# Optimization experiments

Measured on AMD Instinct MI355X. Metric: run time of the kernel, lower is better.

## Reference

```python
import math
import jax, jax.numpy as jnp
import numpy as np

EMBED_LEN = 512  # self.dk in the torch module (used for scaling, NOT the head dim)


def setup_inputs() -> dict:
    key = jax.random.key(0)
    kq, kk, kv = jax.random.split(key, 3)
    B, H, S, D = 2, 8, 4096, 64
    queries = jax.random.normal(kq, (B, H, S, D), dtype=jnp.float32)
    keys = jax.random.normal(kk, (B, H, S, D), dtype=jnp.float32)
    # NOTE: values enters as [B, S, H, D]; forward transposes dims (1,2).
    values = jax.random.normal(kv, (B, S, H, D), dtype=jnp.float32)
    return {"queries": queries, "keys": keys, "values": values}


def reference(queries, keys, values):
    # compatibility = Q @ K^T / sqrt(dk), dk = embed_len (512), mask=None branch
    scores = jnp.einsum("bhqd,bhkd->bhqk", queries, keys) / math.sqrt(EMBED_LEN)
    attn = jax.nn.softmax(scores, axis=3)
    # torch.transpose(values, 1, 2): [B,S,H,D] -> [B,H,S,D]
    v = jnp.swapaxes(values, 1, 2)
    return jnp.einsum("bhqk,bhkd->bhqd", attn, v)
```

## Files before the change

### kernel.cpp

```cpp
#include <hip/hip_runtime.h>

typedef __attribute__((ext_vector_type(8))) short bf16x8;
typedef __attribute__((ext_vector_type(4))) short s16x4;
typedef __attribute__((ext_vector_type(4))) float f32x4;

#define MFMA16 __builtin_amdgcn_mfma_f32_16x16x32_bf16

#if __has_builtin(__builtin_amdgcn_exp2f)
__device__ __forceinline__ float exp2_raw(float x) { return __builtin_amdgcn_exp2f(x); }
#else
__device__ __forceinline__ float exp2_raw(float x) {
    float r;
    asm volatile("v_exp_f32 %0, %1" : "=v"(r) : "v"(x));
    return r;
}
#endif

__device__ __forceinline__ short bf16s(float f) {
    __bf16 h = (__bf16)f;
    return __builtin_bit_cast(short, h);
}

__device__ __forceinline__ void gload16(const char* g, char* l) {
    __builtin_amdgcn_global_load_lds(
        (const __attribute__((address_space(1))) unsigned int*)g,
        (__attribute__((address_space(3))) unsigned int*)l, 16, 0, 0);
}

__global__ __launch_bounds__(256) void prep_k(const float* __restrict__ K,
                                              char* __restrict__ Kimg) {
    const int bid = blockIdx.x;
    const int t = threadIdx.x;
    const int c = t & 3, r = t >> 2;
    char* dst = Kimg + (size_t)bid * 8192;
    const float* src = K + (size_t)bid * 4096 + (size_t)r * 64 + c * 16;
    float e[16];
    *(float4*)(e)      = *(const float4*)(src);
    *(float4*)(e + 4)  = *(const float4*)(src + 4);
    *(float4*)(e + 8)  = *(const float4*)(src + 8);
    *(float4*)(e + 12) = *(const float4*)(src + 12);
#pragma unroll
    for (int lg = 0; lg < 4; ++lg) {
        s16x4 wv;
#pragma unroll
        for (int j = 0; j < 4; ++j) wv[j] = bf16s(e[lg * 4 + j]);
        const unsigned f = (unsigned)((((c >> 1) * 4 + lg) ^ (r & 7)));
        *(s16x4*)(dst + r * 128 + f * 16 + (c & 1) * 8) = wv;
    }
}

__global__ __launch_bounds__(256) void prep_v(const float* __restrict__ V,
                                              char* __restrict__ Vimg) {
    const int bid = blockIdx.x;
    const int head = bid >> 6, it = bid & 63;
    const int b = head >> 3, h = head & 7;
    const int t = threadIdx.x;
    const int d = t & 63, f0 = t >> 6;
    char* dst = Vimg + (size_t)bid * 8192;
#pragma unroll
    for (int ff = 0; ff < 2; ++ff) {
        const int f = f0 + ff * 4;
        const int hh = f >> 2, lg = f & 3;
        const int kv0 = hh * 32 + lg * 4;
        const float* src = V + ((size_t)b * 4096 + it * 64 + kv0) * 512 + h * 64 + d;
        bf16x8 wv;
#pragma unroll
        for (int j = 0; j < 4; ++j) wv[j]     = bf16s(src[(size_t)j * 512]);
#pragma unroll
        for (int j = 0; j < 4; ++j) wv[4 + j] = bf16s(src[(size_t)(16 + j) * 512]);
        *(bf16x8*)(dst + d * 128 + (unsigned)((f ^ (d & 7)) * 16)) = wv;
    }
}

__global__ __launch_bounds__(256, 2)
void sdpa_fa_kernel(const float* __restrict__ Q, const char* __restrict__ Kimg,
                    const char* __restrict__ Vimg, float* __restrict__ O) {
    __shared__ __align__(16) char LDS[65536];

    const int bid  = blockIdx.x;
    const int xcd  = bid & 7;
    const int idx  = bid >> 3;
    const int head = xcd + 8 * (idx >> 5);
    const int qt   = idx & 31;
    const int hb   = head * 64;

    const int t   = threadIdx.x;
    const int w   = t >> 6;
    const int qg  = w >> 1;
    const int kvg = w & 1;
    const int l   = t & 63;
    const int lg  = l >> 4;
    const int lc  = l & 15;
    const int lc7 = lc & 7;

    const float C1 = (float)(1.4426950408889634 / 22.627416997969522);

    bf16x8 qf[4][2];
#pragma unroll
    for (int qi = 0; qi < 4; ++qi) {
        const int qrow = qt * 128 + qg * 64 + qi * 16 + lc;
        const float* qp = Q + ((size_t)head * 4096 + qrow) * 64;
#pragma unroll
        for (int half = 0; half < 2; ++half) {
            bf16x8 f;
#pragma unroll
            for (int j = 0; j < 4; ++j) {
                f[j]     = bf16s(qp[half * 32 + lg * 4 + j] * C1);
                f[4 + j] = bf16s(qp[half * 32 + 16 + lg * 4 + j] * C1);
            }
            qf[qi][half] = f;
        }
    }

    bf16x8 ones;
#pragma unroll
    for (int j = 0; j < 8; ++j) ones[j] = (short)0x3F80;

    f32x4 Oa[4][4];
    f32x4 ls[4];
#pragma unroll
    for (int qi = 0; qi < 4; ++qi) {
        ls[qi] = (f32x4){0.f, 0.f, 0.f, 0.f};
#pragma unroll
        for (int dt = 0; dt < 4; ++dt) Oa[qi][dt] = (f32x4){0.f, 0.f, 0.f, 0.f};
    }

    const char* gimg = (w < 2) ? Kimg : Vimg;
    const char* gbase = gimg + (size_t)(hb + (w & 1)) * 8192 + l * 16;
    auto stage = [&](int it, int buf) {
        const char* g = gbase + (size_t)it * 16384;
        char* lb = LDS + buf * 32768 + w * 8192;
#pragma unroll
        for (int i = 0; i < 8; ++i) gload16(g + i * 1024, lb + i * 1024);
    };

    auto compute = [&](const char* Kb, const char* Vb) {
        bf16x8 kf0[2][2];
#pragma unroll
        for (int g2 = 0; g2 < 2; ++g2) {
            const unsigned ro = (unsigned)((g2 * 16 + lc) * 128);
            kf0[g2][0] = *(const bf16x8*)(Kb + ro + (unsigned)(((0 + lg) ^ lc7) * 16));
            kf0[g2][1] = *(const bf16x8*)(Kb + ro + (unsigned)(((4 + lg) ^ lc7) * 16));
        }
        f32x4 st0[4][2];
#pragma unroll
        for (int g2 = 0; g2 < 2; ++g2)
#pragma unroll
            for (int qi = 0; qi < 4; ++qi) {
                f32x4 a = (f32x4){0.f, 0.f, 0.f, 0.f};
                a = MFMA16(kf0[g2][0], qf[qi][0], a, 0, 0, 0);
                a = MFMA16(kf0[g2][1], qf[qi][1], a, 0, 0, 0);
                st0[qi][g2] = a;
            }

        bf16x8 kf1[2][2];
#pragma unroll
        for (int g2 = 0; g2 < 2; ++g2) {
            const unsigned ro = (unsigned)(((g2 + 2) * 16 + lc) * 128);
            kf1[g2][0] = *(const bf16x8*)(Kb + ro + (unsigned)(((0 + lg) ^ lc7) * 16));
            kf1[g2][1] = *(const bf16x8*)(Kb + ro + (unsigned)(((4 + lg) ^ lc7) * 16));
        }
        f32x4 st1[4][2];
#pragma unroll
        for (int g2 = 0; g2 < 2; ++g2)
#pragma unroll
            for (int qi = 0; qi < 4; ++qi) {
                f32x4 a = (f32x4){0.f, 0.f, 0.f, 0.f};
                a = MFMA16(kf1[g2][0], qf[qi][0], a, 0, 0, 0);
                a = MFMA16(kf1[g2][1], qf[qi][1], a, 0, 0, 0);
                st1[qi][g2] = a;
#pragma unroll
                for (int r = 0; r < 4; ++r) st0[qi][g2][r] = exp2_raw(st0[qi][g2][r]);
            }
        bf16x8 pfr0[4];
#pragma unroll
        for (int qi = 0; qi < 4; ++qi) {
            bf16x8 f;
#pragma unroll
            for (int j = 0; j < 4; ++j) {
                f[j]     = bf16s(st0[qi][0][j]);
                f[4 + j] = bf16s(st0[qi][1][j]);
            }
            pfr0[qi] = f;
        }

        bf16x8 vf[4][2];
#pragma unroll
        for (int dt = 0; dt < 4; ++dt) {
            const unsigned ro = (unsigned)((dt * 16 + lc) * 128);
            vf[dt][0] = *(const bf16x8*)(Vb + ro + (unsigned)(((0 + lg) ^ lc7) * 16));
            vf[dt][1] = *(const bf16x8*)(Vb + ro + (unsigned)(((4 + lg) ^ lc7) * 16));
        }
#pragma unroll
        for (int qi = 0; qi < 4; ++qi) {
            ls[qi] = MFMA16(pfr0[qi], ones, ls[qi], 0, 0, 0);
#pragma unroll
            for (int r = 0; r < 4; ++r) st1[qi][0][r] = exp2_raw(st1[qi][0][r]);
            Oa[qi][0] = MFMA16(pfr0[qi], vf[0][0], Oa[qi][0], 0, 0, 0);
            Oa[qi][1] = MFMA16(pfr0[qi], vf[1][0], Oa[qi][1], 0, 0, 0);
#pragma unroll
            for (int r = 0; r < 4; ++r) st1[qi][1][r] = exp2_raw(st1[qi][1][r]);
            Oa[qi][2] = MFMA16(pfr0[qi], vf[2][0], Oa[qi][2], 0, 0, 0);
            Oa[qi][3] = MFMA16(pfr0[qi], vf[3][0], Oa[qi][3], 0, 0, 0);
        }
        bf16x8 pfr1[4];
#pragma unroll
        for (int qi = 0; qi < 4; ++qi) {
            bf16x8 f;
#pragma unroll
            for (int j = 0; j < 4; ++j) {
                f[j]     = bf16s(st1[qi][0][j]);
                f[4 + j] = bf16s(st1[qi][1][j]);
            }
            pfr1[qi] = f;
        }

#pragma unroll
        for (int qi = 0; qi < 4; ++qi) {
            ls[qi] = MFMA16(pfr1[qi], ones, ls[qi], 0, 0, 0);
#pragma unroll
            for (int dt = 0; dt < 4; ++dt)
                Oa[qi][dt] = MFMA16(pfr1[qi], vf[dt][1], Oa[qi][dt], 0, 0, 0);
        }
    };

    const char* K0 = LDS + kvg * 8192;
    const char* V0 = LDS + 16384 + kvg * 8192;
    const char* K1 = LDS + 32768 + kvg * 8192;
    const char* V1 = LDS + 32768 + 16384 + kvg * 8192;

    stage(0, 0);
    __syncthreads();

#pragma unroll 1
    for (int itp = 0; itp < 16; ++itp) {
        const int it0 = itp * 2;
        stage(it0 + 1, 1);
        compute(K0, V0);
        __syncthreads();
        if (it0 + 2 < 32) stage(it0 + 2, 0);
        compute(K1, V1);
        __syncthreads();
    }

    float* EP = (float*)LDS;
    float* LR = (float*)LDS + 128 * 66;

    if (kvg == 1) {
#pragma unroll
        for (int qi = 0; qi < 4; ++qi) {
#pragma unroll
            for (int dt = 0; dt < 4; ++dt)
#pragma unroll
                for (int r = 0; r < 4; ++r)
                    EP[(qg * 64 + qi * 16 + lg * 4 + r) * 66 + dt * 16 + lc] = Oa[qi][dt][r];
            if (lc == 0)
#pragma unroll
                for (int r = 0; r < 4; ++r) LR[qg * 64 + qi * 16 + lg * 4 + r] = ls[qi][r];
        }
    }
    __syncthreads();
    if (kvg == 0) {
#pragma unroll
        for (int qi = 0; qi < 4; ++qi) {
#pragma unroll
            for (int r = 0; r < 4; ++r) {
                const int qloc = qg * 64 + qi * 16 + lg * 4 + r;
                const float tot = ls[qi][r] + LR[qloc];
                const float inv = 1.0f / tot;
                float* og = O + ((size_t)head * 4096 + qt * 128 + qloc) * 64 + lc;
#pragma unroll
                for (int dt = 0; dt < 4; ++dt)
                    og[dt * 16] = (Oa[qi][dt][r] + EP[qloc * 66 + dt * 16 + lc]) * inv;
            }
        }
    }
}

extern "C" void kernel_launch(void* const* d_in, const int* in_sizes, int n_in,
                              void* d_out, int out_size, void* d_ws, size_t ws_size,
                              hipStream_t stream) {
    const float* Q = (const float*)d_in[0];
    const float* K = (const float*)d_in[1];
    const float* V = (const float*)d_in[2];
    float* Out = (float*)d_out;
    char* Kimg = (char*)d_ws;
    char* Vimg = (char*)d_ws + (size_t)8388608;
    prep_k<<<dim3(1024), dim3(256), 0, stream>>>(K, Kimg);
    prep_v<<<dim3(1024), dim3(256), 0, stream>>>(V, Vimg);
    sdpa_fa_kernel<<<dim3(512), dim3(256), 0, stream>>>(Q, Kimg, Vimg, Out);
}
```

Measured before the change: 85.81 us.

## Use single-wave blocks of 64 queries iterating over all KV tiles

Restructures the attention kernel so each block is one wavefront owning 64 query rows and walking all 64 KV tiles alone, rather than four waves splitting queries and KV halves. This removes the block-wide barriers and the LDS cross-wave reduction of partial outputs and row sums in the epilogue. It uses a per-wave double buffer with explicit vmcnt waits and issues the next tile's loads after the fragment reads. In exchange, each wave loads both K and V tiles itself, so K/V LDS traffic per query roughly doubles, and the launch grows to 1024 blocks.

Result: slower. 91.14 us (+6.2%).

```diff
diff --git a/kernel.cpp b/kernel.cpp
--- a/kernel.cpp
+++ b/kernel.cpp
@@ -72,23 +72,19 @@
     }
 }
 
-__global__ __launch_bounds__(256, 2)
+__global__ __launch_bounds__(64, 2)
 void sdpa_fa_kernel(const float* __restrict__ Q, const char* __restrict__ Kimg,
                     const char* __restrict__ Vimg, float* __restrict__ O) {
-    __shared__ __align__(16) char LDS[65536];
+    __shared__ __align__(16) char LDS[32768];
 
     const int bid  = blockIdx.x;
     const int xcd  = bid & 7;
     const int idx  = bid >> 3;
-    const int head = xcd + 8 * (idx >> 5);
-    const int qt   = idx & 31;
+    const int head = xcd + 8 * (idx >> 6);
+    const int qt   = idx & 63;
     const int hb   = head * 64;
 
-    const int t   = threadIdx.x;
-    const int w   = t >> 6;
-    const int qg  = w >> 1;
-    const int kvg = w & 1;
-    const int l   = t & 63;
+    const int l   = threadIdx.x;
     const int lg  = l >> 4;
     const int lc  = l & 15;
     const int lc7 = lc & 7;
@@ -98,7 +94,7 @@
     bf16x8 qf[4][2];
 #pragma unroll
     for (int qi = 0; qi < 4; ++qi) {
-        const int qrow = qt * 128 + qg * 64 + qi * 16 + lc;
+        const int qrow = qt * 64 + qi * 16 + lc;
         const float* qp = Q + ((size_t)head * 4096 + qrow) * 64;
 #pragma unroll
         for (int half = 0; half < 2; ++half) {
@@ -125,65 +121,28 @@
         for (int dt = 0; dt < 4; ++dt) Oa[qi][dt] = (f32x4){0.f, 0.f, 0.f, 0.f};
     }
 
-    const char* gimg = (w < 2) ? Kimg : Vimg;
-    const char* gbase = gimg + (size_t)(hb + (w & 1)) * 8192 + l * 16;
     auto stage = [&](int it, int buf) {
-        const char* g = gbase + (size_t)it * 16384;
-        char* lb = LDS + buf * 32768 + w * 8192;
-#pragma unroll
-        for (int i = 0; i < 8; ++i) gload16(g + i * 1024, lb + i * 1024);
+        const char* gk = Kimg + (size_t)(hb + it) * 8192 + l * 16;
+        const char* gv = Vimg + (size_t)(hb + it) * 8192 + l * 16;
+        char* lk = LDS + buf * 16384;
+        char* lv = LDS + buf * 16384 + 8192;
+#pragma unroll
+        for (int i = 0; i < 8; ++i) gload16(gk + i * 1024, lk + i * 1024);
+#pragma unroll
+        for (int i = 0; i < 8; ++i) gload16(gv + i * 1024, lv + i * 1024);
     };
 
-    auto compute = [&](const char* Kb, const char* Vb) {
-        bf16x8 kf0[2][2];
-#pragma unroll
-        for (int g2 = 0; g2 < 2; ++g2) {
-            const unsigned ro = (unsigned)((g2 * 16 + lc) * 128);
-            kf0[g2][0] = *(const bf16x8*)(Kb + ro + (unsigned)(((0 + lg) ^ lc7) * 16));
-            kf0[g2][1] = *(const bf16x8*)(Kb + ro + (unsigned)(((4 + lg) ^ lc7) * 16));
-        }
-        f32x4 st0[4][2];
-#pragma unroll
-        for (int g2 = 0; g2 < 2; ++g2)
-#pragma unroll
-            for (int qi = 0; qi < 4; ++qi) {
-                f32x4 a = (f32x4){0.f, 0.f, 0.f, 0.f};
-                a = MFMA16(kf0[g2][0], qf[qi][0], a, 0, 0, 0);
-                a = MFMA16(kf0[g2][1], qf[qi][1], a, 0, 0, 0);
-                st0[qi][g2] = a;
-            }
-
-        bf16x8 kf1[2][2];
-#pragma unroll
-        for (int g2 = 0; g2 < 2; ++g2) {
-            const unsigned ro = (unsigned)(((g2 + 2) * 16 + lc) * 128);
-            kf1[g2][0] = *(const bf16x8*)(Kb + ro + (unsigned)(((0 + lg) ^ lc7) * 16));
-            kf1[g2][1] = *(const bf16x8*)(Kb + ro + (unsigned)(((4 + lg) ^ lc7) * 16));
-        }
-        f32x4 st1[4][2];
-#pragma unroll
-        for (int g2 = 0; g2 < 2; ++g2)
-#pragma unroll
-            for (int qi = 0; qi < 4; ++qi) {
-                f32x4 a = (f32x4){0.f, 0.f, 0.f, 0.f};
-                a = MFMA16(kf1[g2][0], qf[qi][0], a, 0, 0, 0);
-                a = MFMA16(kf1[g2][1], qf[qi][1], a, 0, 0, 0);
-                st1[qi][g2] = a;
-#pragma unroll
-                for (int r = 0; r < 4; ++r) st0[qi][g2][r] = exp2_raw(st0[qi][g2][r]);
-            }
-        bf16x8 pfr0[4];
-#pragma unroll
-        for (int qi = 0; qi < 4; ++qi) {
-            bf16x8 f;
-#pragma unroll
-            for (int j = 0; j < 4; ++j) {
-                f[j]     = bf16s(st0[qi][0][j]);
-                f[4 + j] = bf16s(st0[qi][1][j]);
-            }
-            pfr0[qi] = f;
-        }
-
+    auto body = [&](const char* Kb, const char* Vb, int nextit, int nextbuf) {
+        asm volatile("s_waitcnt vmcnt(0)" ::: "memory");
+        __builtin_amdgcn_sched_barrier(0);
+
+        bf16x8 kf[4][2];
+#pragma unroll
+        for (int g = 0; g < 4; ++g) {
+            const unsigned ro = (unsigned)((g * 16 + lc) * 128);
+            kf[g][0] = *(const bf16x8*)(Kb + ro + (unsigned)(((0 + lg) ^ lc7) * 16));
+            kf[g][1] = *(const bf16x8*)(Kb + ro + (unsigned)(((4 + lg) ^ lc7) * 16));
+        }
         bf16x8 vf[4][2];
 #pragma unroll
         for (int dt = 0; dt < 4; ++dt) {
@@ -191,6 +150,45 @@
             vf[dt][0] = *(const bf16x8*)(Vb + ro + (unsigned)(((0 + lg) ^ lc7) * 16));
             vf[dt][1] = *(const bf16x8*)(Vb + ro + (unsigned)(((4 + lg) ^ lc7) * 16));
         }
+        __builtin_amdgcn_sched_barrier(0);
+
+        if (nextit >= 0) stage(nextit, nextbuf);
+        __builtin_amdgcn_sched_barrier(0);
+
+        f32x4 st0[4][2], st1[4][2];
+#pragma unroll
+        for (int g2 = 0; g2 < 2; ++g2)
+#pragma unroll
+            for (int qi = 0; qi < 4; ++qi) {
+                f32x4 a = (f32x4){0.f, 0.f, 0.f, 0.f};
+                a = MFMA16(kf[g2][0], qf[qi][0], a, 0, 0, 0);
+                a = MFMA16(kf[g2][1], qf[qi][1], a, 0, 0, 0);
+                st0[qi][g2] = a;
+            }
+
+#pragma unroll
+        for (int g2 = 0; g2 < 2; ++g2)
+#pragma unroll
+            for (int qi = 0; qi < 4; ++qi) {
+                f32x4 a = (f32x4){0.f, 0.f, 0.f, 0.f};
+                a = MFMA16(kf[g2 + 2][0], qf[qi][0], a, 0, 0, 0);
+                a = MFMA16(kf[g2 + 2][1], qf[qi][1], a, 0, 0, 0);
+                st1[qi][g2] = a;
+#pragma unroll
+                for (int r = 0; r < 4; ++r) st0[qi][g2][r] = exp2_raw(st0[qi][g2][r]);
+            }
+        bf16x8 pfr0[4];
+#pragma unroll
+        for (int qi = 0; qi < 4; ++qi) {
+            bf16x8 f;
+#pragma unroll
+            for (int j = 0; j < 4; ++j) {
+                f[j]     = bf16s(st0[qi][0][j]);
+                f[4 + j] = bf16s(st0[qi][1][j]);
+            }
+            pfr0[qi] = f;
+        }
+
 #pragma unroll
         for (int qi = 0; qi < 4; ++qi) {
             ls[qi] = MFMA16(pfr0[qi], ones, ls[qi], 0, 0, 0);
@@ -224,55 +222,25 @@
         }
     };
 
-    const char* K0 = LDS + kvg * 8192;
-    const char* V0 = LDS + 16384 + kvg * 8192;
-    const char* K1 = LDS + 32768 + kvg * 8192;
-    const char* V1 = LDS + 32768 + 16384 + kvg * 8192;
-
     stage(0, 0);
-    __syncthreads();
 
 #pragma unroll 1
-    for (int itp = 0; itp < 16; ++itp) {
+    for (int itp = 0; itp < 32; ++itp) {
         const int it0 = itp * 2;
-        stage(it0 + 1, 1);
-        compute(K0, V0);
-        __syncthreads();
-        if (it0 + 2 < 32) stage(it0 + 2, 0);
-        compute(K1, V1);
-        __syncthreads();
-    }
-
-    float* EP = (float*)LDS;
-    float* LR = (float*)LDS + 128 * 66;
-
-    if (kvg == 1) {
-#pragma unroll
-        for (int qi = 0; qi < 4; ++qi) {
-#pragma unroll
-            for (int dt = 0; dt < 4; ++dt)
-#pragma unroll
-                for (int r = 0; r < 4; ++r)
-                    EP[(qg * 64 + qi * 16 + lg * 4 + r) * 66 + dt * 16 + lc] = Oa[qi][dt][r];
-            if (lc == 0)
-#pragma unroll
-                for (int r = 0; r < 4; ++r) LR[qg * 64 + qi * 16 + lg * 4 + r] = ls[qi][r];
-        }
-    }
-    __syncthreads();
-    if (kvg == 0) {
-#pragma unroll
-        for (int qi = 0; qi < 4; ++qi) {
-#pragma unroll
-            for (int r = 0; r < 4; ++r) {
-                const int qloc = qg * 64 + qi * 16 + lg * 4 + r;
-                const float tot = ls[qi][r] + LR[qloc];
-                const float inv = 1.0f / tot;
-                float* og = O + ((size_t)head * 4096 + qt * 128 + qloc) * 64 + lc;
-#pragma unroll
-                for (int dt = 0; dt < 4; ++dt)
-                    og[dt * 16] = (Oa[qi][dt][r] + EP[qloc * 66 + dt * 16 + lc]) * inv;
-            }
+        body(LDS, LDS + 8192, it0 + 1, 1);
+        body(LDS + 16384, LDS + 16384 + 8192,
+             (it0 + 2 < 64) ? (it0 + 2) : -1, 0);
+    }
+
+#pragma unroll
+    for (int qi = 0; qi < 4; ++qi) {
+#pragma unroll
+        for (int r = 0; r < 4; ++r) {
+            const float inv = 1.0f / ls[qi][r];
+            const int q = qt * 64 + qi * 16 + lg * 4 + r;
+            float* og = O + ((size_t)head * 4096 + q) * 64 + lc;
+#pragma unroll
+            for (int dt = 0; dt < 4; ++dt) og[dt * 16] = Oa[qi][dt][r] * inv;
         }
     }
 }
@@ -288,5 +256,5 @@
     char* Vimg = (char*)d_ws + (size_t)8388608;
     prep_k<<<dim3(1024), dim3(256), 0, stream>>>(K, Kimg);
     prep_v<<<dim3(1024), dim3(256), 0, stream>>>(V, Vimg);
-    sdpa_fa_kernel<<<dim3(512), dim3(256), 0, stream>>>(Q, Kimg, Vimg, Out);
-}
+    sdpa_fa_kernel<<<dim3(1024), dim3(64), 0, stream>>>(Q, Kimg, Vimg, Out);
+}
```
